# Optimization experiments

Hardware: AMD Instinct MI355X
Metric: run time of the kernel (lower is better)

## Reference

```python
import jax, jax.numpy as jnp
import numpy as np

N, F, H, CLS = 50000, 64, 128, 64   # nodes, node_features, second_features, num_classes
E, EL = 800000, 200000              # graph edges, decode (label) edges


def setup_inputs() -> dict:
    key = jax.random.key(0)
    ks = jax.random.split(key, 12)
    sc = lambda k, sh, fan: (jax.random.normal(k, sh, jnp.float32) / np.sqrt(fan)).astype(jnp.float32)
    return dict(
        x=jax.random.normal(ks[0], (N, F), jnp.float32),
        edge_index=jax.random.randint(ks[1], (2, E), 0, N),
        edge_label_index=jax.random.randint(ks[2], (2, EL), 0, N),
        hidden1=jnp.zeros((N, H), jnp.float32),   # H state of GCLSTM
        hidden2=jnp.zeros((N, H), jnp.float32),   # C state of GCLSTM
        # GCNConv params
        W_gcn=sc(ks[3], (F, F), F),
        b_gcn=jnp.zeros((F,), jnp.float32),
        # GCLSTM params, gates stacked along last axis in order (i, f, c, o)
        Wx=sc(ks[4], (F, 4 * H), F),      # input->gate weights W_i..W_o
        Th=sc(ks[5], (H, 4 * H), H),      # ChebConv(K=1) thetas on H (pure linear)
        b_gate=jnp.zeros((4 * H,), jnp.float32),  # b_i, b_f, b_c, b_o
        b_conv=jnp.zeros((4 * H,), jnp.float32),  # ChebConv biases
        w_c=sc(ks[6], (3, H), H),         # peephole w_c_i, w_c_f, w_c_o
        # output Linear
        W_lin=sc(ks[7], (H, CLS), H),
        b_lin=jnp.zeros((CLS,), jnp.float32),
    )


def _gcn(x, src, dst, W, b, n):
    """PyG GCNConv: add self-loops, symmetric D^-1/2 (A+I) D^-1/2 normalization."""
    xw = x @ W                                   # [N,F]
    loop = jnp.arange(n)
    src = jnp.concatenate([src, loop])
    dst = jnp.concatenate([dst, loop])
    deg = jax.ops.segment_sum(jnp.ones(src.shape, jnp.float32), dst, num_segments=n)
    dinv = jnp.where(deg > 0, jax.lax.rsqrt(deg), 0.0)
    norm = dinv[src] * dinv[dst]                 # [E+N]
    agg = jax.ops.segment_sum(norm[:, None] * xw[src], dst, num_segments=n)
    return agg + b


def reference(x, edge_index, edge_label_index, hidden1, hidden2,
              W_gcn, b_gcn, Wx, Th, b_gate, b_conv, w_c, W_lin, b_lin):
    n = x.shape[0]
    h = _gcn(x, edge_index[0], edge_index[1], W_gcn, b_gcn, n)   # GCNConv  [N,F]
    # GCLSTM, K=1: ChebConv on H degenerates to H @ Theta + b_conv
    g = (h @ Wx + b_gate) + (hidden1 @ Th + b_conv)              # [N,4H]
    gi, gf, gc, go = jnp.split(g, 4, axis=1)
    I = jax.nn.sigmoid(gi + w_c[0] * hidden2)
    Fg = jax.nn.sigmoid(gf + w_c[1] * hidden2)
    C = Fg * hidden2 + I * jnp.tanh(gc)
    O = jax.nn.sigmoid(go + w_c[2] * C)          # peephole on NEW cell state
    Hn = O * jnp.tanh(C)                         # [N,H]
    z = jax.nn.softmax(jax.nn.relu(Hn) @ W_lin + b_lin, axis=1)  # [N,CLS]
    # decode: dot product of endpoint embeddings
    r = jnp.sum(z[edge_label_index[0]] * z[edge_label_index[1]], axis=-1)  # [EL]
    # faithful to the original forward: returns input hidden1 and the NEW cell state
    return (r, hidden1, C)
```

## Files before the change

kernel.cpp:

```cpp
#include <hip/hip_runtime.h>
#include <math.h>

#define FDIM 64
#define HDIM 128
#define CLSD 64

#define NPART 8
#define MAXDEG 64

typedef unsigned short ushort_t;
typedef _Float16 hfrag __attribute__((ext_vector_type(8)));
typedef float f32x4 __attribute__((ext_vector_type(4)));

#define LOG2E 1.4426950408889634f

__device__ __forceinline__ float ex2(float x){ float r; asm("v_exp_f32 %0, %1" : "=v"(r) : "v"(x)); return r; }
__device__ __forceinline__ float rcp_(float x){ float r; asm("v_rcp_f32 %0, %1" : "=v"(r) : "v"(x)); return r; }
__device__ __forceinline__ float fsigmoid(float x){ return rcp_(1.0f + ex2(-LOG2E*x)); }
__device__ __forceinline__ float ftanh(float x){ return 1.0f - 2.0f*rcp_(1.0f + ex2(2.0f*LOG2E*x)); }

__device__ __forceinline__ ushort_t f2h(float f){
    _Float16 h = (_Float16)f;
    ushort_t u; __builtin_memcpy(&u, &h, 2); return u;
}
__device__ __forceinline__ float hflo(unsigned int u){
    ushort_t v = (ushort_t)u; _Float16 h; __builtin_memcpy(&h, &v, 2); return (float)h;
}
__device__ __forceinline__ float hfhi(unsigned int u){
    ushort_t v = (ushort_t)(u >> 16); _Float16 h; __builtin_memcpy(&h, &v, 2); return (float)h;
}
__device__ __forceinline__ unsigned int pk2h(float a, float b){
    return (unsigned int)f2h(a) | ((unsigned int)f2h(b) << 16);
}


__launch_bounds__(256)
__global__ void k_pre(const float* __restrict__ x,  const float* __restrict__ Wg,
                      const float* __restrict__ bg,
                      const float* __restrict__ Wx, const float* __restrict__ Th,
                      const float* __restrict__ Wl,
                      const float* __restrict__ bga, const float* __restrict__ bco,
                      const float* __restrict__ h1,
                      ushort_t* __restrict__ Bh, ushort_t* __restrict__ Lh,
                      float* __restrict__ bsum, int* __restrict__ cnt,
                      ushort_t* __restrict__ xh, ushort_t* __restrict__ Ab,
                      float* __restrict__ oh1, int N, int N2){
    int tid = blockIdx.x*256 + threadIdx.x;
    const int secW = 107008 + N;
    const int secX = secW + N*8;
    if (tid < 98304){
        int k = tid >> 9, col = tid & 511;
        float v;
        if (k < 64){
            float acc = 0.f;
            #pragma unroll 8
            for (int f = 0; f < 64; ++f) acc += Wg[k*64 + f]*Wx[f*512 + col];
            v = acc;
        } else {
            v = Th[(k-64)*512 + col];
        }
        int g = col >> 7, hc = col & 127;
        int w = hc >> 5, within = hc & 31;
        int c8 = g*2 + (within >> 4);
        int T = w*8 + c8;
        int s = k >> 5;
        int lane = ((k >> 3) & 3)*16 + (within & 15);
        int pos = ((T*6 + s)*64 + lane)*8 + (k & 7);
        Bh[pos] = f2h(v);
    } else if (tid < 106496){
        int i = tid - 98304;
        int k = i >> 6, col = i & 63;
        float v = Wl[k*64 + col];
        int ct = col >> 4;
        int s = k >> 5;
        int lane = ((k >> 3) & 3)*16 + (col & 15);
        int pos = ((ct*4 + s)*64 + lane)*8 + (k & 7);
        Lh[pos] = f2h(v);
    } else if (tid < 107008){
        int c = tid - 106496;
        float acc = bga[c] + bco[c];
        #pragma unroll 8
        for (int f = 0; f < 64; ++f) acc += bg[f]*Wx[f*512 + c];
        bsum[c] = acc;
    } else if (tid < secW){
        cnt[tid - 107008] = 0;
    } else if (tid < secX){
        int i = tid - secW;
        const float4* xp = (const float4*)(x + (size_t)i*8);
        float4 p0 = xp[0], p1 = xp[1];
        ((int4*)xh)[i] = make_int4((int)pk2h(p0.x,p0.y), (int)pk2h(p0.z,p0.w),
                                   (int)pk2h(p1.x,p1.y), (int)pk2h(p1.z,p1.w));
    } else {
        int i = tid - secX;
        if (i >= N2*16) return;
        int n = i >> 4, q = i & 15;
        int4 frag = make_int4(0,0,0,0);
        if (n < N){
            const float4* src = (const float4*)(h1 + (size_t)n*128 + q*8);
            float4 p0 = src[0], p1 = src[1];
            float4* dst = (float4*)(oh1 + (size_t)n*128 + q*8);
            dst[0] = p0; dst[1] = p1;
            frag = make_int4((int)pk2h(p0.x,p0.y), (int)pk2h(p0.z,p0.w),
                             (int)pk2h(p1.x,p1.y), (int)pk2h(p1.z,p1.w));
        }
        int s = 2 + (q >> 2);
        int lane = (q & 3)*16 + (n & 15);
        ((int4*)Ab)[((size_t)(n >> 4)*6 + s)*64 + lane] = frag;
    }
}

__launch_bounds__(256)
__global__ void k_fill(const int* __restrict__ ei, int* __restrict__ cnt,
                       int* __restrict__ ell, int E, int psz){
    int p   = blockIdx.x % NPART;
    int bi  = blockIdx.x / NPART;
    int bpp = gridDim.x / NPART;
    int chunk = (E + bpp - 1) / bpp;
    int beg = bi*chunk;
    int end = beg + chunk; if (end > E) end = E;
    int lo = p*psz, hi = lo + psz;
    for (int i = beg + threadIdx.x; i < end; i += 256){
        int d = ei[E + i];
        if (d >= lo && d < hi){
            int s = ei[i];
            int slot = atomicAdd(&cnt[d], 1);
            if (slot < MAXDEG) ell[(size_t)d*MAXDEG + slot] = s;
        }
    }
}

__launch_bounds__(256)
__global__ void k_dinv(const int* __restrict__ cnt, float* __restrict__ dinv, int N){
    int i = blockIdx.x*256 + threadIdx.x;
    if (i < N) dinv[i] = rsqrtf((float)cnt[i] + 1.0f);
}

__launch_bounds__(256)
__global__ void k_gather(const int* __restrict__ cnt, const int* __restrict__ ell,
                         const float* __restrict__ dinv, const ushort_t* __restrict__ xh,
                         ushort_t* __restrict__ Ab, int N, int N2){
    int tid = blockIdx.x*256 + threadIdx.x;
    int n = tid >> 3, q = tid & 7;
    if (n >= N2) return;
    int s_ = q >> 2;
    int lane = (q & 3)*16 + (n & 15);
    size_t fpos = ((size_t)(n >> 4)*6 + s_)*64 + lane;
    if (n >= N){
        ((int4*)Ab)[fpos] = make_int4(0,0,0,0);
        return;
    }
    int cn = cnt[n]; if (cn > MAXDEG) cn = MAXDEG;
    const int* row = ell + (size_t)n*MAXDEG;
    const int4* xv = (const int4*)xh;
    float a0=0.f,a1=0.f,a2=0.f,a3=0.f,a4=0.f,a5=0.f,a6=0.f,a7=0.f;
    int idx = 0;
    for (; idx + 4 <= cn; idx += 4){
        int s0 = row[idx], s1 = row[idx+1], s2 = row[idx+2], s3 = row[idx+3];
        float w0 = dinv[s0], w1 = dinv[s1], w2 = dinv[s2], w3 = dinv[s3];
        int4 u = xv[(size_t)s0*8 + q];
        int4 p = xv[(size_t)s1*8 + q];
        int4 v = xv[(size_t)s2*8 + q];
        int4 z = xv[(size_t)s3*8 + q];
        a0 += w0*hflo((unsigned)u.x) + w1*hflo((unsigned)p.x) + w2*hflo((unsigned)v.x) + w3*hflo((unsigned)z.x);
        a1 += w0*hfhi((unsigned)u.x) + w1*hfhi((unsigned)p.x) + w2*hfhi((unsigned)v.x) + w3*hfhi((unsigned)z.x);
        a2 += w0*hflo((unsigned)u.y) + w1*hflo((unsigned)p.y) + w2*hflo((unsigned)v.y) + w3*hflo((unsigned)z.y);
        a3 += w0*hfhi((unsigned)u.y) + w1*hfhi((unsigned)p.y) + w2*hfhi((unsigned)v.y) + w3*hfhi((unsigned)z.y);
        a4 += w0*hflo((unsigned)u.z) + w1*hflo((unsigned)p.z) + w2*hflo((unsigned)v.z) + w3*hflo((unsigned)z.z);
        a5 += w0*hfhi((unsigned)u.z) + w1*hfhi((unsigned)p.z) + w2*hfhi((unsigned)v.z) + w3*hfhi((unsigned)z.z);
        a6 += w0*hflo((unsigned)u.w) + w1*hflo((unsigned)p.w) + w2*hflo((unsigned)v.w) + w3*hflo((unsigned)z.w);
        a7 += w0*hfhi((unsigned)u.w) + w1*hfhi((unsigned)p.w) + w2*hfhi((unsigned)v.w) + w3*hfhi((unsigned)z.w);
    }
    for (; idx < cn; ++idx){
        int s0 = row[idx];
        float w0 = dinv[s0];
        int4 u = xv[(size_t)s0*8 + q];
        a0 += w0*hflo((unsigned)u.x); a1 += w0*hfhi((unsigned)u.x);
        a2 += w0*hflo((unsigned)u.y); a3 += w0*hfhi((unsigned)u.y);
        a4 += w0*hflo((unsigned)u.z); a5 += w0*hfhi((unsigned)u.z);
        a6 += w0*hflo((unsigned)u.w); a7 += w0*hfhi((unsigned)u.w);
    }
    float dn = dinv[n];
    int4 sv = xv[(size_t)n*8 + q];
    a0 = dn*(a0 + dn*hflo((unsigned)sv.x));
    a1 = dn*(a1 + dn*hfhi((unsigned)sv.x));
    a2 = dn*(a2 + dn*hflo((unsigned)sv.y));
    a3 = dn*(a3 + dn*hfhi((unsigned)sv.y));
    a4 = dn*(a4 + dn*hflo((unsigned)sv.z));
    a5 = dn*(a5 + dn*hfhi((unsigned)sv.z));
    a6 = dn*(a6 + dn*hflo((unsigned)sv.w));
    a7 = dn*(a7 + dn*hfhi((unsigned)sv.w));
    ((int4*)Ab)[fpos] = make_int4((int)pk2h(a0,a1), (int)pk2h(a2,a3),
                                  (int)pk2h(a4,a5), (int)pk2h(a6,a7));
}

__launch_bounds__(512)
__global__ void k_fused(const ushort_t* __restrict__ Ab, const float* __restrict__ h2,
                        const ushort_t* __restrict__ Bh, const ushort_t* __restrict__ Lh,
                        const float* __restrict__ bsum, const float* __restrict__ wc,
                        const float* __restrict__ blin,
                        float* __restrict__ outC, ushort_t* __restrict__ zb, int N)
{
    __shared__ __align__(16) char smem[33792];
    ushort_t* Hh   = (ushort_t*)smem;
    float*    Ltile = (float*)(smem + 16384);

    const int t    = threadIdx.x;
    const int w    = t >> 6;
    const int wm   = w >> 2;
    const int wn   = w & 3;
    const int lane = t & 63;
    const int nb   = blockIdx.x * 64;
    const size_t bt = (size_t)blockIdx.x * 4;

    f32x4 acc[2][8];
    #pragma unroll
    for (int mt = 0; mt < 2; ++mt)
        #pragma unroll
        for (int c8 = 0; c8 < 8; ++c8)
            acc[mt][c8] = (f32x4){0.f,0.f,0.f,0.f};

    const hfrag* AF  = (const hfrag*)Ab;
    const hfrag* BhF = (const hfrag*)Bh;

    #pragma unroll
    for (int s = 0; s < 6; ++s){
        hfrag a0 = AF[((bt + wm*2 + 0)*6 + s)*64 + lane];
        hfrag a1 = AF[((bt + wm*2 + 1)*6 + s)*64 + lane];
        #pragma unroll
        for (int c8 = 0; c8 < 8; ++c8){
            int T = wn*8 + c8;
            hfrag bh = BhF[(T*6 + s)*64 + lane];
            acc[0][c8] = __builtin_amdgcn_mfma_f32_16x16x32_f16(a0, bh, acc[0][c8], 0,0,0);
            acc[1][c8] = __builtin_amdgcn_mfma_f32_16x16x32_f16(a1, bh, acc[1][c8], 0,0,0);
        }
    }

    #pragma unroll
    for (int hc_t = 0; hc_t < 2; ++hc_t){
        int hc  = wn*32 + hc_t*16 + (lane & 15);
        float bi = bsum[hc],       bfv = bsum[128 + hc];
        float bc = bsum[256 + hc], bo  = bsum[384 + hc];
        float wci = wc[hc], wcf = wc[128 + hc], wco = wc[256 + hc];
        #pragma unroll
        for (int mt = 0; mt < 2; ++mt){
            #pragma unroll
            for (int rr = 0; rr < 4; ++rr){
                int row = wm*32 + mt*16 + ((lane >> 4) & 3)*4 + rr;
                int gr  = nb + row;
                float gi = acc[mt][0 + hc_t][rr] + bi;
                float gf = acc[mt][2 + hc_t][rr] + bfv;
                float gc = acc[mt][4 + hc_t][rr] + bc;
                float go = acc[mt][6 + hc_t][rr] + bo;
                float hv = (gr < N) ? h2[(size_t)gr*128 + hc] : 0.0f;
                float I  = fsigmoid(gi + wci*hv);
                float Fg = fsigmoid(gf + wcf*hv);
                float C  = Fg*hv + I*ftanh(gc);
                float O  = fsigmoid(go + wco*C);
                float hn = O*ftanh(C);
                if (gr < N) outC[(size_t)gr*128 + hc] = C;
                float hr = fmaxf(hn, 0.0f);
                int l2  = (row & 15) + (hc_t*2 + ((lane >> 3) & 1))*16;
                int pos = (((wm*2 + mt)*4 + wn)*64 + l2)*8 + (lane & 7);
                Hh[pos] = f2h(hr);
            }
        }
    }
    __syncthreads();

    const hfrag* HF  = (const hfrag*)Hh;
    const hfrag* LhF = (const hfrag*)Lh;
    f32x4 acc2[2];
    acc2[0] = (f32x4){0.f,0.f,0.f,0.f};
    acc2[1] = (f32x4){0.f,0.f,0.f,0.f};
    #pragma unroll
    for (int sp = 0; sp < 4; ++sp){
        hfrag a0 = HF[((wm*2+0)*4 + sp)*64 + lane];
        hfrag a1 = HF[((wm*2+1)*4 + sp)*64 + lane];
        hfrag bh = LhF[(wn*4 + sp)*64 + lane];
        acc2[0] = __builtin_amdgcn_mfma_f32_16x16x32_f16(a0, bh, acc2[0], 0,0,0);
        acc2[1] = __builtin_amdgcn_mfma_f32_16x16x32_f16(a1, bh, acc2[1], 0,0,0);
    }
    {
        int cls = wn*16 + (lane & 15);
        float bv = blin[cls];
        #pragma unroll
        for (int mtl = 0; mtl < 2; ++mtl){
            #pragma unroll
            for (int rr = 0; rr < 4; ++rr){
                int row = wm*32 + mtl*16 + ((lane >> 4) & 3)*4 + rr;
                Ltile[row*68 + cls] = acc2[mtl][rr] + bv;
            }
        }
    }
    __syncthreads();

    {
        int m = t >> 3, q = t & 7;
        const float4* Lr = (const float4*)&Ltile[m*68 + q*8];
        float4 v0 = Lr[0], v1 = Lr[1];
        float mx = fmaxf(fmaxf(fmaxf(v0.x,v0.y),fmaxf(v0.z,v0.w)),
                         fmaxf(fmaxf(v1.x,v1.y),fmaxf(v1.z,v1.w)));
        #pragma unroll
        for (int off2 = 1; off2 < 8; off2 <<= 1) mx = fmaxf(mx, __shfl_xor(mx, off2, 64));
        float e[8];
        e[0]=ex2(LOG2E*(v0.x-mx)); e[1]=ex2(LOG2E*(v0.y-mx));
        e[2]=ex2(LOG2E*(v0.z-mx)); e[3]=ex2(LOG2E*(v0.w-mx));
        e[4]=ex2(LOG2E*(v1.x-mx)); e[5]=ex2(LOG2E*(v1.y-mx));
        e[6]=ex2(LOG2E*(v1.z-mx)); e[7]=ex2(LOG2E*(v1.w-mx));
        float s8 = e[0]+e[1]+e[2]+e[3]+e[4]+e[5]+e[6]+e[7];
        #pragma unroll
        for (int off2 = 1; off2 < 8; off2 <<= 1) s8 += __shfl_xor(s8, off2, 64);
        float inv = rcp_(s8);
        if (nb + m < N){
            ((int4*)zb)[(size_t)(nb+m)*8 + q] =
                make_int4((int)pk2h(e[0]*inv, e[1]*inv), (int)pk2h(e[2]*inv, e[3]*inv),
                          (int)pk2h(e[4]*inv, e[5]*inv), (int)pk2h(e[6]*inv, e[7]*inv));
        }
    }
}

__launch_bounds__(256)
__global__ void k_dec(const int* __restrict__ eli, const ushort_t* __restrict__ zb,
                      float* __restrict__ r, int EL){
    int tid = blockIdx.x*256 + threadIdx.x;
    int e = tid >> 3, l = tid & 7;
    if (e >= EL) return;
    int s = eli[e], d = eli[EL + e];
    int4 a = ((const int4*)zb)[(size_t)s*8 + l];
    int4 b = ((const int4*)zb)[(size_t)d*8 + l];
    unsigned int ua[4] = {(unsigned)a.x,(unsigned)a.y,(unsigned)a.z,(unsigned)a.w};
    unsigned int ub[4] = {(unsigned)b.x,(unsigned)b.y,(unsigned)b.z,(unsigned)b.w};
    float p = 0.f;
    #pragma unroll
    for (int j = 0; j < 4; ++j){
        p += hflo(ua[j])*hflo(ub[j]) + hfhi(ua[j])*hfhi(ub[j]);
    }
    #pragma unroll
    for (int off = 1; off < 8; off <<= 1) p += __shfl_xor(p, off, 64);
    if (l == 0) r[e] = p;
}

extern "C" void kernel_launch(void* const* d_in, const int* in_sizes, int n_in,
                              void* d_out, int out_size, void* d_ws, size_t ws_size,
                              hipStream_t stream)
{
    const float* x   = (const float*)d_in[0];
    const int*   ei  = (const int*)  d_in[1];
    const int*   eli = (const int*)  d_in[2];
    const float* h1  = (const float*)d_in[3];
    const float* h2  = (const float*)d_in[4];
    const float* Wg  = (const float*)d_in[5];
    const float* bg  = (const float*)d_in[6];
    const float* Wx  = (const float*)d_in[7];
    const float* Th  = (const float*)d_in[8];
    const float* bga = (const float*)d_in[9];
    const float* bco = (const float*)d_in[10];
    const float* wc  = (const float*)d_in[11];
    const float* Wl  = (const float*)d_in[12];
    const float* bl  = (const float*)d_in[13];

    const int N  = in_sizes[0] / FDIM;
    const int E  = in_sizes[1] / 2;
    const int EL = in_sizes[2] / 2;
    const int N2 = (N + 63) & ~63;
    const int PSZ = (N + NPART - 1) / NPART;

    float* ws   = (float*)d_ws;
    ushort_t* xh = (ushort_t*)ws;
    ushort_t* Ab = xh + (size_t)N*64;
    ushort_t* zb = Ab + (size_t)N2*192;
    float* dinv = (float*)(zb + (size_t)N*64);
    int*   cnt  = (int*)(dinv + N);
    int*   ell  = cnt + N;
    size_t base = (size_t)((ell + (size_t)N*MAXDEG) - (int*)ws);
    base = (base + 3) & ~(size_t)3;
    ushort_t* Bh = (ushort_t*)(ws + base);
    ushort_t* Lh = Bh + 98304;
    float*  bsum = (float*)(Lh + 8192);

    float* out = (float*)d_out;
    float* r   = out;
    float* oh1 = out + EL;
    float* oC  = out + EL + (size_t)N*HDIM;

    const int preThreads = 107008 + N + N*8 + N2*16;
    const int epBlocks   = NPART * 256;
    k_pre   <<<(preThreads + 255)/256, 256, 0, stream>>>(x, Wg, bg, Wx, Th, Wl, bga, bco,
                                                         h1, Bh, Lh, bsum, cnt,
                                                         xh, Ab, oh1, N, N2);
    k_fill  <<<epBlocks, 256, 0, stream>>>(ei, cnt, ell, E, PSZ);
    k_dinv  <<<(N + 255)/256, 256, 0, stream>>>(cnt, dinv, N);
    k_gather<<<((size_t)N2*8 + 255)/256, 256, 0, stream>>>(cnt, ell, dinv, xh, Ab, N, N2);
    k_fused <<<N2/64, 512, 0, stream>>>(Ab, h2, Bh, Lh, bsum, wc, bl, oC, zb, N);
    k_dec   <<<(EL*8 + 255)/256, 256, 0, stream>>>(eli, zb, r, EL);
}
```

Baseline: 121.0 us.

## Split prep kernel, fold dinv into gather, prefetch A fragments in fused GEMM

Splits the prep kernel into a weight-packing kernel and an activation-conversion kernel, and replaces the in-kernel zeroing of cnt with a memset. Removes the k_dinv launch and its buffer by computing rsqrt of degree inline in the gather. Changes the B-fragment layout to be s-major and software-prefetches the next A fragment in the fused GEMM loop, with explicit B loads per step. This trades one launch and a dinv round trip for recomputing rsqrt per edge, and adds a memset and one extra launch.

```diff
diff --git a/kernel.cpp b/kernel.cpp
--- a/kernel.cpp
+++ b/kernel.cpp
@@ -35,19 +35,13 @@
 
 
 __launch_bounds__(256)
-__global__ void k_pre(const float* __restrict__ x,  const float* __restrict__ Wg,
-                      const float* __restrict__ bg,
-                      const float* __restrict__ Wx, const float* __restrict__ Th,
-                      const float* __restrict__ Wl,
-                      const float* __restrict__ bga, const float* __restrict__ bco,
-                      const float* __restrict__ h1,
-                      ushort_t* __restrict__ Bh, ushort_t* __restrict__ Lh,
-                      float* __restrict__ bsum, int* __restrict__ cnt,
-                      ushort_t* __restrict__ xh, ushort_t* __restrict__ Ab,
-                      float* __restrict__ oh1, int N, int N2){
+__global__ void k_preW(const float* __restrict__ Wg, const float* __restrict__ bg,
+                       const float* __restrict__ Wx, const float* __restrict__ Th,
+                       const float* __restrict__ Wl,
+                       const float* __restrict__ bga, const float* __restrict__ bco,
+                       ushort_t* __restrict__ Bh, ushort_t* __restrict__ Lh,
+                       float* __restrict__ bsum){
     int tid = blockIdx.x*256 + threadIdx.x;
-    const int secW = 107008 + N;
-    const int secX = secW + N*8;
     if (tid < 98304){
         int k = tid >> 9, col = tid & 511;
         float v;
@@ -65,7 +59,7 @@
         int T = w*8 + c8;
         int s = k >> 5;
         int lane = ((k >> 3) & 3)*16 + (within & 15);
-        int pos = ((T*6 + s)*64 + lane)*8 + (k & 7);
+        int pos = ((s*32 + T)*64 + lane)*8 + (k & 7);
         Bh[pos] = f2h(v);
     } else if (tid < 106496){
         int i = tid - 98304;
@@ -82,16 +76,21 @@
         #pragma unroll 8
         for (int f = 0; f < 64; ++f) acc += bg[f]*Wx[f*512 + c];
         bsum[c] = acc;
-    } else if (tid < secW){
-        cnt[tid - 107008] = 0;
-    } else if (tid < secX){
-        int i = tid - secW;
-        const float4* xp = (const float4*)(x + (size_t)i*8);
+    }
+}
+
+__launch_bounds__(256)
+__global__ void k_preX(const float* __restrict__ x, const float* __restrict__ h1,
+                       ushort_t* __restrict__ xh, ushort_t* __restrict__ Ab,
+                       float* __restrict__ oh1, int N, int N2){
+    int tid = blockIdx.x*256 + threadIdx.x;
+    if (tid < N*8){
+        const float4* xp = (const float4*)(x + (size_t)tid*8);
         float4 p0 = xp[0], p1 = xp[1];
-        ((int4*)xh)[i] = make_int4((int)pk2h(p0.x,p0.y), (int)pk2h(p0.z,p0.w),
-                                   (int)pk2h(p1.x,p1.y), (int)pk2h(p1.z,p1.w));
+        ((int4*)xh)[tid] = make_int4((int)pk2h(p0.x,p0.y), (int)pk2h(p0.z,p0.w),
+                                     (int)pk2h(p1.x,p1.y), (int)pk2h(p1.z,p1.w));
     } else {
-        int i = tid - secX;
+        int i = tid - N*8;
         if (i >= N2*16) return;
         int n = i >> 4, q = i & 15;
         int4 frag = make_int4(0,0,0,0);
@@ -130,14 +129,8 @@
 }
 
 __launch_bounds__(256)
-__global__ void k_dinv(const int* __restrict__ cnt, float* __restrict__ dinv, int N){
-    int i = blockIdx.x*256 + threadIdx.x;
-    if (i < N) dinv[i] = rsqrtf((float)cnt[i] + 1.0f);
-}
-
-__launch_bounds__(256)
 __global__ void k_gather(const int* __restrict__ cnt, const int* __restrict__ ell,
-                         const float* __restrict__ dinv, const ushort_t* __restrict__ xh,
+                         const ushort_t* __restrict__ xh,
                          ushort_t* __restrict__ Ab, int N, int N2){
     int tid = blockIdx.x*256 + threadIdx.x;
     int n = tid >> 3, q = tid & 7;
@@ -156,7 +149,10 @@
     int idx = 0;
     for (; idx + 4 <= cn; idx += 4){
         int s0 = row[idx], s1 = row[idx+1], s2 = row[idx+2], s3 = row[idx+3];
-        float w0 = dinv[s0], w1 = dinv[s1], w2 = dinv[s2], w3 = dinv[s3];
+        float w0 = rsqrtf((float)cnt[s0] + 1.0f);
+        float w1 = rsqrtf((float)cnt[s1] + 1.0f);
+        float w2 = rsqrtf((float)cnt[s2] + 1.0f);
+        float w3 = rsqrtf((float)cnt[s3] + 1.0f);
         int4 u = xv[(size_t)s0*8 + q];
         int4 p = xv[(size_t)s1*8 + q];
         int4 v = xv[(size_t)s2*8 + q];
@@ -172,14 +168,14 @@
     }
     for (; idx < cn; ++idx){
         int s0 = row[idx];
-        float w0 = dinv[s0];
+        float w0 = rsqrtf((float)cnt[s0] + 1.0f);
         int4 u = xv[(size_t)s0*8 + q];
         a0 += w0*hflo((unsigned)u.x); a1 += w0*hfhi((unsigned)u.x);
         a2 += w0*hflo((unsigned)u.y); a3 += w0*hfhi((unsigned)u.y);
         a4 += w0*hflo((unsigned)u.z); a5 += w0*hfhi((unsigned)u.z);
         a6 += w0*hflo((unsigned)u.w); a7 += w0*hfhi((unsigned)u.w);
     }
-    float dn = dinv[n];
+    float dn = rsqrtf((float)cn + 1.0f);
     int4 sv = xv[(size_t)n*8 + q];
     a0 = dn*(a0 + dn*hflo((unsigned)sv.x));
     a1 = dn*(a1 + dn*hfhi((unsigned)sv.x));
@@ -222,17 +218,45 @@
     const hfrag* AF  = (const hfrag*)Ab;
     const hfrag* BhF = (const hfrag*)Bh;
 
+    const size_t aidx0 = (bt + wm*2 + 0)*384 + lane;
+    const size_t aidx1 = (bt + wm*2 + 1)*384 + lane;
+    const size_t bb    = (size_t)(wn*8)*64 + lane;
+
+    hfrag a0 = AF[aidx0];
+    hfrag a1 = AF[aidx1];
     #pragma unroll
     for (int s = 0; s < 6; ++s){
-        hfrag a0 = AF[((bt + wm*2 + 0)*6 + s)*64 + lane];
-        hfrag a1 = AF[((bt + wm*2 + 1)*6 + s)*64 + lane];
-        #pragma unroll
-        for (int c8 = 0; c8 < 8; ++c8){
-            int T = wn*8 + c8;
-            hfrag bh = BhF[(T*6 + s)*64 + lane];
-            acc[0][c8] = __builtin_amdgcn_mfma_f32_16x16x32_f16(a0, bh, acc[0][c8], 0,0,0);
-            acc[1][c8] = __builtin_amdgcn_mfma_f32_16x16x32_f16(a1, bh, acc[1][c8], 0,0,0);
-        }
+        size_t sb = (size_t)s*2048 + bb;
+        hfrag b0 = BhF[sb +   0];
+        hfrag b1 = BhF[sb +  64];
+        hfrag b2 = BhF[sb + 128];
+        hfrag b3 = BhF[sb + 192];
+        hfrag b4 = BhF[sb + 256];
+        hfrag b5 = BhF[sb + 320];
+        hfrag b6 = BhF[sb + 384];
+        hfrag b7 = BhF[sb + 448];
+        hfrag a0n = a0, a1n = a1;
+        if (s < 5){
+            a0n = AF[aidx0 + (s+1)*64];
+            a1n = AF[aidx1 + (s+1)*64];
+        }
+        acc[0][0] = __builtin_amdgcn_mfma_f32_16x16x32_f16(a0, b0, acc[0][0], 0,0,0);
+        acc[1][0] = __builtin_amdgcn_mfma_f32_16x16x32_f16(a1, b0, acc[1][0], 0,0,0);
+        acc[0][1] = __builtin_amdgcn_mfma_f32_16x16x32_f16(a0, b1, acc[0][1], 0,0,0);
+        acc[1][1] = __builtin_amdgcn_mfma_f32_16x16x32_f16(a1, b1, acc[1][1], 0,0,0);
+        acc[0][2] = __builtin_amdgcn_mfma_f32_16x16x32_f16(a0, b2, acc[0][2], 0,0,0);
+        acc[1][2] = __builtin_amdgcn_mfma_f32_16x16x32_f16(a1, b2, acc[1][2], 0,0,0);
+        acc[0][3] = __builtin_amdgcn_mfma_f32_16x16x32_f16(a0, b3, acc[0][3], 0,0,0);
+        acc[1][3] = __builtin_amdgcn_mfma_f32_16x16x32_f16(a1, b3, acc[1][3], 0,0,0);
+        acc[0][4] = __builtin_amdgcn_mfma_f32_16x16x32_f16(a0, b4, acc[0][4], 0,0,0);
+        acc[1][4] = __builtin_amdgcn_mfma_f32_16x16x32_f16(a1, b4, acc[1][4], 0,0,0);
+        acc[0][5] = __builtin_amdgcn_mfma_f32_16x16x32_f16(a0, b5, acc[0][5], 0,0,0);
+        acc[1][5] = __builtin_amdgcn_mfma_f32_16x16x32_f16(a1, b5, acc[1][5], 0,0,0);
+        acc[0][6] = __builtin_amdgcn_mfma_f32_16x16x32_f16(a0, b6, acc[0][6], 0,0,0);
+        acc[1][6] = __builtin_amdgcn_mfma_f32_16x16x32_f16(a1, b6, acc[1][6], 0,0,0);
+        acc[0][7] = __builtin_amdgcn_mfma_f32_16x16x32_f16(a0, b7, acc[0][7], 0,0,0);
+        acc[1][7] = __builtin_amdgcn_mfma_f32_16x16x32_f16(a1, b7, acc[1][7], 0,0,0);
+        a0 = a0n; a1 = a1n;
     }
 
     #pragma unroll
@@ -274,11 +298,11 @@
     acc2[1] = (f32x4){0.f,0.f,0.f,0.f};
     #pragma unroll
     for (int sp = 0; sp < 4; ++sp){
-        hfrag a0 = HF[((wm*2+0)*4 + sp)*64 + lane];
-        hfrag a1 = HF[((wm*2+1)*4 + sp)*64 + lane];
-        hfrag bh = LhF[(wn*4 + sp)*64 + lane];
-        acc2[0] = __builtin_amdgcn_mfma_f32_16x16x32_f16(a0, bh, acc2[0], 0,0,0);
-        acc2[1] = __builtin_amdgcn_mfma_f32_16x16x32_f16(a1, bh, acc2[1], 0,0,0);
+        hfrag a0l = HF[((wm*2+0)*4 + sp)*64 + lane];
+        hfrag a1l = HF[((wm*2+1)*4 + sp)*64 + lane];
+        hfrag bh  = LhF[(wn*4 + sp)*64 + lane];
+        acc2[0] = __builtin_amdgcn_mfma_f32_16x16x32_f16(a0l, bh, acc2[0], 0,0,0);
+        acc2[1] = __builtin_amdgcn_mfma_f32_16x16x32_f16(a1l, bh, acc2[1], 0,0,0);
     }
     {
         int cls = wn*16 + (lane & 15);
@@ -369,8 +393,7 @@
     ushort_t* xh = (ushort_t*)ws;
     ushort_t* Ab = xh + (size_t)N*64;
     ushort_t* zb = Ab + (size_t)N2*192;
-    float* dinv = (float*)(zb + (size_t)N*64);
-    int*   cnt  = (int*)(dinv + N);
+    int*   cnt  = (int*)(zb + (size_t)N*64);
     int*   ell  = cnt + N;
     size_t base = (size_t)((ell + (size_t)N*MAXDEG) - (int*)ws);
     base = (base + 3) & ~(size_t)3;
@@ -383,14 +406,15 @@
     float* oh1 = out + EL;
     float* oC  = out + EL + (size_t)N*HDIM;
 
-    const int preThreads = 107008 + N + N*8 + N2*16;
-    const int epBlocks   = NPART * 256;
-    k_pre   <<<(preThreads + 255)/256, 256, 0, stream>>>(x, Wg, bg, Wx, Th, Wl, bga, bco,
-                                                         h1, Bh, Lh, bsum, cnt,
-                                                         xh, Ab, oh1, N, N2);
+    const int epBlocks  = NPART * 256;
+    const int pXthreads = N*8 + N2*16;
+
+    hipMemsetAsync(cnt, 0, (size_t)N*sizeof(int), stream);
+    k_preW  <<<(107008 + 255)/256, 256, 0, stream>>>(Wg, bg, Wx, Th, Wl, bga, bco,
+                                                     Bh, Lh, bsum);
+    k_preX  <<<(pXthreads + 255)/256, 256, 0, stream>>>(x, h1, xh, Ab, oh1, N, N2);
     k_fill  <<<epBlocks, 256, 0, stream>>>(ei, cnt, ell, E, PSZ);
-    k_dinv  <<<(N + 255)/256, 256, 0, stream>>>(cnt, dinv, N);
-    k_gather<<<((size_t)N2*8 + 255)/256, 256, 0, stream>>>(cnt, ell, dinv, xh, Ab, N, N2);
+    k_gather<<<((size_t)N2*8 + 255)/256, 256, 0, stream>>>(cnt, ell, xh, Ab, N, N2);
     k_fused <<<N2/64, 512, 0, stream>>>(Ab, h2, Bh, Lh, bsum, wc, bl, oC, zb, N);
     k_dec   <<<(EL*8 + 255)/256, 256, 0, stream>>>(eli, zb, r, EL);
 }
```

Measured after the change: 129.9 us. 7.4% more time.
